# Kernel tuning notes

Hardware: AMD Instinct MI355X
Metric: run time of the kernel (lower is better)

The kernel has to match this reference:

```python
import itertools
import jax, jax.numpy as jnp
import numpy as np

EPS = 1e-15
B, K, H, W = 64, 8, 128, 128


def setup_inputs() -> dict:
    key = jax.random.key(0)
    k1, k2 = jax.random.split(key)
    pred_masks = jax.random.uniform(k1, (B, K, H, W), dtype=jnp.float32)
    aug_masks = jax.random.uniform(k2, (B, K, H, W), dtype=jnp.float32)
    return {"pred_masks": pred_masks, "aug_masks": aug_masks}


def _mask_kl_div(pred, true):
    # true * (log(true+eps) - log(pred+eps)), mean over (H, W)
    return (true * (jnp.log(true + EPS) - jnp.log(pred + EPS))).mean(axis=(-2, -1))


# all K! permutations, precomputed once (K=8 -> 40320 perms)
_PERMS = jnp.asarray(np.array(list(itertools.permutations(range(K))), dtype=np.int32))


def reference(pred_masks, aug_masks):
    b, k, h, w = pred_masks.shape
    t = aug_masks  # targets are detached in torch for the cost matrix
    # Fused pairwise KL cost matrix (avoids the (B,K,K,H,W) broadcast):
    # C[b,i,j] = mean_hw[ t_j*log(t_j+eps) ] - mean_hw[ t_j*log(p_i+eps) ]
    ent = (t * jnp.log(t + EPS)).mean(axis=(-2, -1))          # (B, K) over j
    cross = jnp.einsum('bjhw,bihw->bij', t, jnp.log(pred_masks + EPS)) / (h * w)
    C = ent[:, None, :] - cross                                # (B, K, K)
    # exact linear assignment via exhaustive search over K! permutations
    rows = jnp.arange(k)
    costs = C[:, rows[None, :], _PERMS].sum(axis=-1)           # (B, K!)
    R2C = _PERMS[jnp.argmin(costs, axis=1)]                    # (B, K) col for each row
    # permute rows: out[b, i] = pred[b, argsort(R2C)[b, i]]
    row_perm = jnp.argsort(R2C, axis=1)
    pred_perm = jnp.take_along_axis(pred_masks, row_perm[:, :, None, None], axis=1)
    l = _mask_kl_div(pred_perm, t)                             # (B, K)
    return l.mean(), pred_perm[..., None]
```

## Files before the change

### kernel.cpp

```cpp
#include <hip/hip_runtime.h>


#define BB 64
#define KK 8
#define HW 16384
#define CH 64
#define CHUNK 256
#define EPSF 1e-15f

struct MaskTab {
    unsigned char masks[255];
    int off[9];
};

constexpr MaskTab make_tab() {
    MaskTab t{};
    int idx = 0;
    for (int p = 1; p <= 8; ++p) {
        t.off[p - 1] = idx;
        for (int m = 1; m < 256; ++m) {
            int c = 0;
            for (int b = 0; b < 8; ++b) c += (m >> b) & 1;
            if (c == p) t.masks[idx++] = (unsigned char)m;
        }
    }
    t.off[8] = idx;
    return t;
}

__constant__ MaskTab kTab = make_tab();

__device__ __forceinline__ float dot4(float4 t, float4 l) {
    return t.x * l.x + t.y * l.y + t.z * l.z + t.w * l.w;
}

__device__ __forceinline__ float4 log4(float4 a) {
    float4 r;
    r.x = __logf(a.x + EPSF); r.y = __logf(a.y + EPSF);
    r.z = __logf(a.z + EPSF); r.w = __logf(a.w + EPSF);
    return r;
}

__global__ __launch_bounds__(256) void cost_kernel(const float* __restrict__ pred,
                                                   const float* __restrict__ aug,
                                                   float* __restrict__ part)
{
    __shared__ float tile[16][CHUNK];

    const int blk   = blockIdx.x;
    const int b     = blk >> 6;
    const int chunk = blk & 63;
    const int tid   = threadIdx.x;
    const int wave  = tid >> 6;
    const int lane  = tid & 63;

    const size_t base = (size_t)b * (KK * HW) + (size_t)chunk * CHUNK;

#pragma unroll
    for (int m = 0; m < 4; ++m) {
        const int vr = wave + 4 * m;
        const float* g = ((vr < 8) ? (pred + base + (size_t)vr * HW)
                                   : (aug  + base + (size_t)(vr - 8) * HW)) + lane * 4;
        __builtin_amdgcn_global_load_lds(
            (const __attribute__((address_space(1))) void*)g,
            (__attribute__((address_space(3))) void*)&tile[vr][lane * 4],
            16, 0, 0);
    }
    __syncthreads();

    const int w2 = 2 * wave;
    const int e4 = lane * 4;

    const float4 p0 = *(const float4*)&tile[w2][e4];
    const float4 p1 = *(const float4*)&tile[w2 + 1][e4];
    const float4 la = log4(p0);
    const float4 lc = log4(p1);
    const float4 t0 = *(const float4*)&tile[8 + w2][e4];
    const float4 t1 = *(const float4*)&tile[8 + w2 + 1][e4];
    float e0 = dot4(t0, log4(t0));
    float e1 = dot4(t1, log4(t1));

    float acc[16];
#pragma unroll
    for (int j = 0; j < 8; ++j) {
        const float4 tv = *(const float4*)&tile[8 + j][e4];
        acc[j]     = dot4(tv, la);
        acc[8 + j] = dot4(tv, lc);
    }

#pragma unroll
    for (int v = 0; v < 16; ++v) {
        float s = acc[v];
#pragma unroll
        for (int d = 1; d < 64; d <<= 1) s += __shfl_xor(s, d);
        acc[v] = s;
    }
#pragma unroll
    for (int d = 1; d < 64; d <<= 1) e0 += __shfl_xor(e0, d);
#pragma unroll
    for (int d = 1; d < 64; d <<= 1) e1 += __shfl_xor(e1, d);

    if (lane == 0) {
        float* dst = part + (size_t)blk * 72;
#pragma unroll
        for (int j = 0; j < 8; ++j) {
            dst[16 * wave + j]     = acc[j];
            dst[16 * wave + 8 + j] = acc[8 + j];
        }
        dst[64 + w2]     = e0;
        dst[64 + w2 + 1] = e1;
    }
}

__global__ __launch_bounds__(256) void permute_kernel(const float* __restrict__ pred,
                                                      const float* __restrict__ part,
                                                      float* __restrict__ out)
{
    __shared__ float red[72];
    __shared__ float C[64];
    __shared__ float dp[256];
    __shared__ int   choice[256];
    __shared__ int   inv8[8];

    const int g    = blockIdx.x;
    const int p    = g >> 1;
    const int half = g & 1;
    const int b    = p >> 3;
    const int tid  = threadIdx.x;

    const float* pb = part + (size_t)b * CH * 72;
    if (tid < 72) {
        float s = 0.f;
#pragma unroll
        for (int c = 0; c < CH; ++c) s += pb[c * 72 + tid];
        red[tid] = s;
    }
    __syncthreads();
    if (tid < 64) C[tid] = red[64 + (tid & 7)] - red[tid];
    if (tid == 0) dp[0] = 0.f;
    __syncthreads();

    const int grp = tid >> 3;
    const int j   = tid & 7;

    for (int lvl = 1; lvl <= 8; ++lvl) {
        const int start = kTab.off[lvl - 1];
        const int end   = kTab.off[lvl];
        const float* Crow = &C[(lvl - 1) * 8];
        for (int base = start; base < end; base += 32) {
            const int mi = base + grp;
            if (mi < end) {
                const int M = kTab.masks[mi];
                float v  = 1e30f;
                int   bj = 0;
                if (M & (1 << j)) {
                    v  = dp[M ^ (1 << j)] + Crow[j];
                    bj = j;
                }
#pragma unroll
                for (int d = 1; d < 8; d <<= 1) {
                    float ov = __shfl_xor(v, d);
                    int   oj = __shfl_xor(bj, d);
                    if (ov < v) { v = ov; bj = oj; }
                }
                if (j == 0) { dp[M] = v; choice[M] = bj; }
            }
        }
        __syncthreads();
    }

    if (tid == 0) {
        int mask = 255;
        for (int r = 7; r >= 0; --r) {
            const int jj = choice[mask];
            inv8[jj] = r;
            mask ^= 1 << jj;
        }
        if (g == (b << 4))
            atomicAdd(out, dp[255] * (1.0f / (16384.0f * 512.0f)));
    }
    __syncthreads();

    const int src_row = inv8[p & 7];
    const float* src = pred + ((size_t)(b << 3) + src_row) * HW;
    float*       drow = out + 1 + (size_t)p * HW;

#pragma unroll
    for (int m = 0; m < 8; ++m) {
        const int f = half * 2048 + tid + 256 * m;
        const int e = 3 + 4 * f;
        if (f < 4095) {
            float4 v;
            v.x = src[e]; v.y = src[e + 1]; v.z = src[e + 2]; v.w = src[e + 3];
            *(float4*)(drow + e) = v;
        } else {
            drow[0] = src[0]; drow[1] = src[1]; drow[2] = src[2];
            drow[16383] = src[16383];
        }
    }
}

extern "C" void kernel_launch(void* const* d_in, const int* in_sizes, int n_in,
                              void* d_out, int out_size, void* d_ws, size_t ws_size,
                              hipStream_t stream) {
    const float* pred = (const float*)d_in[0];
    const float* aug  = (const float*)d_in[1];
    float* out = (float*)d_out;
    float* part = (float*)d_ws;

    hipMemsetAsync(d_out, 0, sizeof(float), stream);

    cost_kernel<<<dim3(BB * CH), dim3(256), 0, stream>>>(pred, aug, part);
    permute_kernel<<<dim3(1024), dim3(256), 0, stream>>>(pred, part, out);
}
```

Baseline: 129.6 us.

## Split assignment into per-batch kernel and drop redundant DP from permute blocks

Before, each of 1024 permute blocks redundantly reduced partials and ran the subset DP for its batch. Now a separate 64-block, single-wave kernel does this once per batch and writes the inverse permutation and per-batch loss to workspace. The copy kernel uses 2048 blocks that only gather rows, and block 0 sums the losses, which removes the memset and the atomic. This adds a third launch and an extra dependency between kernels.

```diff
diff --git a/kernel.cpp b/kernel.cpp
--- a/kernel.cpp
+++ b/kernel.cpp
@@ -112,42 +112,39 @@
     }
 }
 
-__global__ __launch_bounds__(256) void permute_kernel(const float* __restrict__ pred,
-                                                      const float* __restrict__ part,
-                                                      float* __restrict__ out)
+__global__ __launch_bounds__(64) void assign_kernel(const float* __restrict__ part,
+                                                    int* __restrict__ ws_inv,
+                                                    float* __restrict__ ws_loss)
 {
-    __shared__ float red[72];
     __shared__ float C[64];
     __shared__ float dp[256];
     __shared__ int   choice[256];
-    __shared__ int   inv8[8];
-
-    const int g    = blockIdx.x;
-    const int p    = g >> 1;
-    const int half = g & 1;
-    const int b    = p >> 3;
-    const int tid  = threadIdx.x;
-
+
+    const int b    = blockIdx.x;
+    const int lane = threadIdx.x;
     const float* pb = part + (size_t)b * CH * 72;
-    if (tid < 72) {
-        float s = 0.f;
-#pragma unroll
-        for (int c = 0; c < CH; ++c) s += pb[c * 72 + tid];
-        red[tid] = s;
-    }
+
+    float s = 0.f;
+#pragma unroll 8
+    for (int c = 0; c < CH; ++c) s += pb[c * 72 + lane];
+    float e = 0.f;
+    if (lane < 8) {
+#pragma unroll 8
+        for (int c = 0; c < CH; ++c) e += pb[c * 72 + 64 + lane];
+    }
+    const float entj = __shfl(e, lane & 7);
+    C[lane] = entj - s;
+    if (lane == 0) dp[0] = 0.f;
     __syncthreads();
-    if (tid < 64) C[tid] = red[64 + (tid & 7)] - red[tid];
-    if (tid == 0) dp[0] = 0.f;
-    __syncthreads();
-
-    const int grp = tid >> 3;
-    const int j   = tid & 7;
-
-    for (int lvl = 1; lvl <= 8; ++lvl) {
-        const int start = kTab.off[lvl - 1];
-        const int end   = kTab.off[lvl];
-        const float* Crow = &C[(lvl - 1) * 8];
-        for (int base = start; base < end; base += 32) {
+
+    const int grp = lane >> 3;
+    const int j   = lane & 7;
+
+    for (int p = 1; p <= 8; ++p) {
+        const int start = kTab.off[p - 1];
+        const int end   = kTab.off[p];
+        const float* Crow = &C[(p - 1) * 8];
+        for (int base = start; base < end; base += 8) {
             const int mi = base + grp;
             if (mi < end) {
                 const int M = kTab.masks[mi];
@@ -159,8 +156,8 @@
                 }
 #pragma unroll
                 for (int d = 1; d < 8; d <<= 1) {
-                    float ov = __shfl_xor(v, d);
-                    int   oj = __shfl_xor(bj, d);
+                    const float ov = __shfl_xor(v, d);
+                    const int   oj = __shfl_xor(bj, d);
                     if (ov < v) { v = ov; bj = oj; }
                 }
                 if (j == 0) { dp[M] = v; choice[M] = bj; }
@@ -169,25 +166,35 @@
         __syncthreads();
     }
 
-    if (tid == 0) {
+    if (lane == 0) {
         int mask = 255;
         for (int r = 7; r >= 0; --r) {
             const int jj = choice[mask];
-            inv8[jj] = r;
+            ws_inv[b * 8 + jj] = r;
             mask ^= 1 << jj;
         }
-        if (g == (b << 4))
-            atomicAdd(out, dp[255] * (1.0f / (16384.0f * 512.0f)));
-    }
-    __syncthreads();
-
-    const int src_row = inv8[p & 7];
+        ws_loss[b] = dp[255] * (1.0f / (16384.0f * 512.0f));
+    }
+}
+
+__global__ __launch_bounds__(256) void permute_kernel(const float* __restrict__ pred,
+                                                      const int* __restrict__ ws_inv,
+                                                      const float* __restrict__ ws_loss,
+                                                      float* __restrict__ out)
+{
+    const int blk  = blockIdx.x;
+    const int pair = blk >> 2;
+    const int q    = blk & 3;
+    const int b    = pair >> 3;
+    const int tid  = threadIdx.x;
+
+    const int src_row = ws_inv[pair];
     const float* src = pred + ((size_t)(b << 3) + src_row) * HW;
-    float*       drow = out + 1 + (size_t)p * HW;
-
-#pragma unroll
-    for (int m = 0; m < 8; ++m) {
-        const int f = half * 2048 + tid + 256 * m;
+    float*      drow = out + 1 + (size_t)pair * HW;
+
+#pragma unroll
+    for (int m = 0; m < 4; ++m) {
+        const int f = q * 1024 + tid + 256 * m;
         const int e = 3 + 4 * f;
         if (f < 4095) {
             float4 v;
@@ -198,6 +205,13 @@
             drow[16383] = src[16383];
         }
     }
+
+    if (blk == 0 && tid < 64) {
+        float v = ws_loss[tid];
+#pragma unroll
+        for (int d = 1; d < 64; d <<= 1) v += __shfl_xor(v, d);
+        if (tid == 0) out[0] = v;
+    }
 }
 
 extern "C" void kernel_launch(void* const* d_in, const int* in_sizes, int n_in,
@@ -206,10 +220,12 @@
     const float* pred = (const float*)d_in[0];
     const float* aug  = (const float*)d_in[1];
     float* out = (float*)d_out;
-    float* part = (float*)d_ws;
-
-    hipMemsetAsync(d_out, 0, sizeof(float), stream);
+
+    float* part    = (float*)d_ws;
+    int*   ws_inv  = (int*)(part + BB * CH * 72);
+    float* ws_loss = (float*)(ws_inv + BB * KK);
 
     cost_kernel<<<dim3(BB * CH), dim3(256), 0, stream>>>(pred, aug, part);
-    permute_kernel<<<dim3(1024), dim3(256), 0, stream>>>(pred, part, out);
-}
+    assign_kernel<<<dim3(BB), dim3(64), 0, stream>>>(part, ws_inv, ws_loss);
+    permute_kernel<<<dim3(2048), dim3(256), 0, stream>>>(pred, ws_inv, ws_loss, out);
+}
```

New measurement: 137.3 us. +6.0%, slower.
